# Kernel tuning notes

Measured on AMD Instinct MI355X. Metric: run time of the kernel, lower is better.

Reference implementation:

```python
import jax, jax.numpy as jnp
import numpy as np

EPS = 1e-5

def _layernorm(x, w, b):
    mu = jnp.mean(x, axis=-1, keepdims=True)
    var = jnp.mean(jnp.square(x - mu), axis=-1, keepdims=True)
    return (x - mu) * jax.lax.rsqrt(var + EPS) * w + b

def setup_inputs() -> dict:
    key = jax.random.key(0)
    ks = jax.random.split(key, 8)
    B, N, NH, F_IN, F_OUT = 1, 196608, 9, 64, 64
    x = jax.random.normal(ks[0], (B, N, F_IN), dtype=jnp.float32)
    adjc = jax.random.randint(ks[1], (N, NH), 0, N, dtype=jnp.int64)
    # NHConv layer weights: contract over (neighborhood, features)
    s1 = 1.0 / np.sqrt(NH * F_IN)
    s2 = 1.0 / np.sqrt(NH * F_OUT)
    W1 = jax.random.normal(ks[2], (NH, F_IN, F_OUT), dtype=jnp.float32) * s1
    b1 = jnp.zeros((F_OUT,), dtype=jnp.float32)
    W2 = jax.random.normal(ks[3], (NH, F_OUT, F_OUT), dtype=jnp.float32) * s2
    b2 = jnp.zeros((F_OUT,), dtype=jnp.float32)
    ln1_w = jnp.ones((F_IN,), dtype=jnp.float32)
    ln1_b = jnp.zeros((F_IN,), dtype=jnp.float32)
    ln2_w = jnp.ones((F_OUT,), dtype=jnp.float32)
    ln2_b = jnp.zeros((F_OUT,), dtype=jnp.float32)
    return {"x": x, "adjc": adjc, "ln1_w": ln1_w, "ln1_b": ln1_b,
            "W1": W1, "b1": b1, "ln2_w": ln2_w, "ln2_b": ln2_b,
            "W2": W2, "b2": b2}

def reference(x, adjc, ln1_w, ln1_b, W1, b1, ln2_w, ln2_b, W2, b2):
    # skip_layer: identity since in_features == out_features
    x_res = x
    # block 1: norm -> SiLU -> neighborhood gather -> per-node linear
    h = jax.nn.silu(_layernorm(x, ln1_w, ln1_b))
    h_nh = h[:, adjc, :]                      # [B, N, nh, F_in]
    h = jnp.einsum('bnkf,kfo->bno', h_nh, W1) + b1
    # block 2
    h = jax.nn.silu(_layernorm(h, ln2_w, ln2_b))
    h_nh = h[:, adjc, :]                      # [B, N, nh, F_out]
    h = jnp.einsum('bnkf,kfo->bno', h_nh, W2) + b2
    return h + x_res
```

## Files before the change

### kernel.cpp

```cpp
#include <hip/hip_runtime.h>

#define NNODES 196608
#define NH 9
#define F 64
#define K_TOT 576
#define KSTEPS 18
#define LN_EPS 1e-5f

typedef __attribute__((ext_vector_type(8))) short short8v;
typedef __attribute__((ext_vector_type(4))) float f32x4;

__device__ __forceinline__ unsigned short f2bf(float f) {
    unsigned int u = __float_as_uint(f);
    u += 0x7fff + ((u >> 16) & 1);
    return (unsigned short)(u >> 16);
}
__device__ __forceinline__ float bf2f(unsigned short u) {
    return __uint_as_float((unsigned int)u << 16);
}
__device__ __forceinline__ float silu_f(float z) { return z / (1.0f + __expf(-z)); }

__device__ __forceinline__ void gload_lds16(const void* g, void* l) {
    __builtin_amdgcn_global_load_lds((__attribute__((address_space(1))) void*)g,
                                     (__attribute__((address_space(3))) void*)l,
                                     16, 0, 0);
}

__global__ __launch_bounds__(256) void prep_wt(const float* __restrict__ W1,
                                               const float* __restrict__ W2,
                                               unsigned short* __restrict__ Wt1,
                                               unsigned short* __restrict__ Wt2) {
    int tid = blockIdx.x * 256 + threadIdx.x;
    if (tid >= F * K_TOT) return;
    int o = tid & 63, k = tid >> 6;
    int s = k >> 5, lg = (k & 31) >> 3, j = k & 7;
    int w = o >> 4, l16 = o & 15;
    int dst = ((s * 4 + w) * 64 + lg * 16 + l16) * 8 + j;
    Wt1[dst] = f2bf(W1[(size_t)k * F + o]);
    Wt2[dst] = f2bf(W2[(size_t)k * F + o]);
}

__global__ __launch_bounds__(256) void ln1_silu(const float* __restrict__ x,
                                                const float* __restrict__ w,
                                                const float* __restrict__ b,
                                                unsigned short* __restrict__ out,
                                                unsigned short* __restrict__ xbf) {
    const int t = threadIdx.x;
    const int row = blockIdx.x * 16 + (t >> 4);
    const int fl = (t & 15) * 4;
    const float4 v = *(const float4*)(x + (size_t)row * F + fl);
    float s = v.x + v.y + v.z + v.w;
    float ss = v.x * v.x + v.y * v.y + v.z * v.z + v.w * v.w;
#pragma unroll
    for (int o = 8; o; o >>= 1) { s += __shfl_xor(s, o); ss += __shfl_xor(ss, o); }
    const float mu = s * (1.0f / F);
    const float rstd = rsqrtf(ss * (1.0f / F) - mu * mu + LN_EPS);
    const float4 wv = *(const float4*)(w + fl);
    const float4 bv = *(const float4*)(b + fl);
    ushort4 o4;
    o4.x = f2bf(silu_f((v.x - mu) * rstd * wv.x + bv.x));
    o4.y = f2bf(silu_f((v.y - mu) * rstd * wv.y + bv.y));
    o4.z = f2bf(silu_f((v.z - mu) * rstd * wv.z + bv.z));
    o4.w = f2bf(silu_f((v.w - mu) * rstd * wv.w + bv.w));
    *(ushort4*)(out + (size_t)row * F + fl) = o4;
    if (xbf) {
        ushort4 xq;
        xq.x = f2bf(v.x); xq.y = f2bf(v.y); xq.z = f2bf(v.z); xq.w = f2bf(v.w);
        *(ushort4*)(xbf + (size_t)row * F + fl) = xq;
    }
}

template<int FINAL, int XBF>
__global__ __launch_bounds__(256) __attribute__((amdgpu_waves_per_eu(3, 4)))
void gconv_mfma(
    const unsigned short* __restrict__ h,
    const int* __restrict__ adjc,
    const unsigned short* __restrict__ Wt,
    const float* __restrict__ bias,
    const float* __restrict__ lnw, const float* __restrict__ lnb,
    const void* __restrict__ xres,
    void* __restrict__ outv)
{
    __shared__ __align__(16) char smem[4 * 8192];
    unsigned short* tile = (unsigned short*)smem;
    float (*T)[68] = (float (*)[68])smem;

    const int wave = threadIdx.x >> 6;
    const int lane = threadIdx.x & 63;
    const int l16 = lane & 15, lg = lane >> 4;
    const int nodeBase = blockIdx.x * 64;

    const int srow = lane >> 3;
    const int sswz = (lane & 7) ^ srow;
    const int rA = wave * 16 + srow;
    const int rB = rA + 8;

    int idxA[NH], idxB[NH];
    {
        const int* a0 = adjc + (size_t)(nodeBase + rA) * NH;
        const int* a1 = adjc + (size_t)(nodeBase + rB) * NH;
#pragma unroll
        for (int hh = 0; hh < NH; ++hh) { idxA[hh] = a0[hh]; idxB[hh] = a1[hh]; }
    }

    short8v bfrag[KSTEPS];
    {
        const short8v* wp = (const short8v*)(Wt) + (size_t)wave * 64 + lane;
#pragma unroll
        for (int s = 0; s < KSTEPS; ++s) bfrag[s] = wp[(size_t)s * 256];
    }
#pragma unroll
    for (int s = 0; s < KSTEPS; ++s)
        asm volatile("" : "+v"(bfrag[s]));

    f32x4 acc[4];
#pragma unroll
    for (int m = 0; m < 4; ++m) acc[m] = (f32x4){0.f, 0.f, 0.f, 0.f};

#define STAGE(BUF, HH)                                                         \
    do {                                                                       \
        gload_lds16(h + (size_t)idxA[HH] * F + sswz * 8,                       \
                    (char*)tile + (BUF) * 8192 + (2 * wave) * 1024);           \
        gload_lds16(h + (size_t)idxB[HH] * F + sswz * 8,                       \
                    (char*)tile + (BUF) * 8192 + (2 * wave + 1) * 1024);       \
    } while (0)

#define COMPUTE(BUF, HH)                                                       \
    _Pragma("unroll")                                                          \
    for (int m = 0; m < 4; ++m) {                                              \
        _Pragma("unroll")                                                      \
        for (int kh = 0; kh < 2; ++kh) {                                       \
            const short8v a = *(const short8v*)((char*)tile + (BUF) * 8192     \
                + (m * 16 + l16) * 128 + (((kh * 4 + lg) ^ (l16 & 7)) * 16));  \
            acc[m] = __builtin_amdgcn_mfma_f32_16x16x32_bf16(                  \
                a, bfrag[(HH) * 2 + kh], acc[m], 0, 0, 0);                     \
        }                                                                      \
    }

    STAGE(0, 0);
    STAGE(1, 1);
    STAGE(2, 2);
#pragma unroll
    for (int hh = 0; hh < NH; ++hh) {
        if (hh <= NH - 3)      { asm volatile("s_waitcnt vmcnt(4)" ::: "memory"); }
        else if (hh == NH - 2) { asm volatile("s_waitcnt vmcnt(2)" ::: "memory"); }
        else                   { asm volatile("s_waitcnt vmcnt(0)" ::: "memory"); }
        __builtin_amdgcn_s_barrier();
        if (hh < NH - 3) STAGE((hh + 3) & 3, hh + 3);
        COMPUTE(hh & 3, hh);
    }
#undef STAGE
#undef COMPUTE

    __syncthreads();

#pragma unroll
    for (int m = 0; m < 4; ++m)
#pragma unroll
        for (int r = 0; r < 4; ++r)
            T[m * 16 + lg * 4 + r][wave * 16 + l16] = acc[m][r];
    __syncthreads();

    const int t = threadIdx.x;
    const int nl = t >> 2, q = t & 3;
    const int node = nodeBase + nl;
    float v[16];
#pragma unroll
    for (int i = 0; i < 16; ++i) v[i] = T[nl][q * 16 + i] + bias[q * 16 + i];

    if (FINAL) {
        float* out = (float*)outv;
        if (XBF) {
            const unsigned short* xb = (const unsigned short*)xres;
            unsigned short xr[16];
            *(short8v*)(xr)     = *(const short8v*)(xb + (size_t)node * F + q * 16);
            *(short8v*)(xr + 8) = *(const short8v*)(xb + (size_t)node * F + q * 16 + 8);
#pragma unroll
            for (int i4 = 0; i4 < 4; ++i4) {
                float4 ov;
                ov.x = v[i4 * 4 + 0] + bf2f(xr[i4 * 4 + 0]);
                ov.y = v[i4 * 4 + 1] + bf2f(xr[i4 * 4 + 1]);
                ov.z = v[i4 * 4 + 2] + bf2f(xr[i4 * 4 + 2]);
                ov.w = v[i4 * 4 + 3] + bf2f(xr[i4 * 4 + 3]);
                *(float4*)(out + (size_t)node * F + q * 16 + i4 * 4) = ov;
            }
        } else {
            const float* xf = (const float*)xres;
#pragma unroll
            for (int i4 = 0; i4 < 4; ++i4) {
                const float4 xv = *(const float4*)(xf + (size_t)node * F + q * 16 + i4 * 4);
                float4 ov;
                ov.x = v[i4 * 4 + 0] + xv.x; ov.y = v[i4 * 4 + 1] + xv.y;
                ov.z = v[i4 * 4 + 2] + xv.z; ov.w = v[i4 * 4 + 3] + xv.w;
                *(float4*)(out + (size_t)node * F + q * 16 + i4 * 4) = ov;
            }
        }
    } else {
        float s = 0.f, ss = 0.f;
#pragma unroll
        for (int i = 0; i < 16; ++i) { s += v[i]; ss += v[i] * v[i]; }
        s += __shfl_xor(s, 1); ss += __shfl_xor(ss, 1);
        s += __shfl_xor(s, 2); ss += __shfl_xor(ss, 2);
        const float mu = s * (1.0f / F);
        const float rstd = rsqrtf(ss * (1.0f / F) - mu * mu + LN_EPS);
        unsigned short* out = (unsigned short*)outv;
        unsigned short ob[16];
#pragma unroll
        for (int i = 0; i < 16; ++i) {
            const int o = q * 16 + i;
            const float y = (v[i] - mu) * rstd * lnw[o] + lnb[o];
            ob[i] = f2bf(silu_f(y));
        }
#pragma unroll
        for (int c = 0; c < 2; ++c)
            *(short8v*)(out + (size_t)node * F + q * 16 + c * 8) = *(short8v*)(ob + c * 8);
    }
}

extern "C" void kernel_launch(void* const* d_in, const int* in_sizes, int n_in,
                              void* d_out, int out_size, void* d_ws, size_t ws_size,
                              hipStream_t stream)
{
    const float* x    = (const float*)d_in[0];
    const int*   adjc = (const int*)d_in[1];
    const float* ln1w = (const float*)d_in[2];
    const float* ln1b = (const float*)d_in[3];
    const float* W1   = (const float*)d_in[4];
    const float* b1   = (const float*)d_in[5];
    const float* ln2w = (const float*)d_in[6];
    const float* ln2b = (const float*)d_in[7];
    const float* W2   = (const float*)d_in[8];
    const float* b2   = (const float*)d_in[9];
    float* out = (float*)d_out;

    const size_t hElems = (size_t)NNODES * F;
    unsigned short* h1  = (unsigned short*)d_ws;
    unsigned short* h2  = h1 + hElems;
    unsigned short* Wt1 = h2 + hElems;
    unsigned short* Wt2 = Wt1 + F * K_TOT;
    unsigned short* xbf = Wt2 + F * K_TOT;
    const size_t need = (3 * hElems + 2 * (size_t)F * K_TOT) * sizeof(unsigned short);
    const bool useXbf = ws_size >= need;

    prep_wt<<<(F * K_TOT + 255) / 256, 256, 0, stream>>>(W1, W2, Wt1, Wt2);
    ln1_silu<<<NNODES / 16, 256, 0, stream>>>(x, ln1w, ln1b, h1, useXbf ? xbf : nullptr);
    gconv_mfma<0, 0><<<NNODES / 64, 256, 0, stream>>>(h1, adjc, Wt1, b1, ln2w, ln2b, nullptr, h2);
    if (useXbf)
        gconv_mfma<1, 1><<<NNODES / 64, 256, 0, stream>>>(h2, adjc, Wt2, b2, nullptr, nullptr, xbf, out);
    else
        gconv_mfma<1, 0><<<NNODES / 64, 256, 0, stream>>>(h2, adjc, Wt2, b2, nullptr, nullptr, x, out);
}
```

Before: 108.6 us.

## Make each wave compute all output columns for its own 16 nodes without block barriers

Each wave now owns a private LDS region and 16 nodes, and computes all four 16-column output tiles itself, so the block-wide barriers in the gather loop go away. Weight fragments are no longer held in registers for the whole kernel; they are double-buffered per neighbor from global memory, interleaved with a four-deep gather pipeline driven by explicit vmcnt waits. The epilogue reads the MFMA accumulators directly and does the LayerNorm reduction with 16-lane shuffles, which drops the LDS transpose. In exchange, every wave re-reads the full weight matrix per neighbor, and the output writes become narrow scalar stores instead of vector stores. The waves-per-EU hint is also pinned to 3.

```diff
diff --git a/kernel.cpp b/kernel.cpp
--- a/kernel.cpp
+++ b/kernel.cpp
@@ -4,7 +4,6 @@
 #define NH 9
 #define F 64
 #define K_TOT 576
-#define KSTEPS 18
 #define LN_EPS 1e-5f
 
 typedef __attribute__((ext_vector_type(8))) short short8v;
@@ -71,7 +70,7 @@
 }
 
 template<int FINAL, int XBF>
-__global__ __launch_bounds__(256) __attribute__((amdgpu_waves_per_eu(3, 4)))
+__global__ __launch_bounds__(256) __attribute__((amdgpu_waves_per_eu(3, 3)))
 void gconv_mfma(
     const unsigned short* __restrict__ h,
     const int* __restrict__ adjc,
@@ -82,138 +81,127 @@
     void* __restrict__ outv)
 {
     __shared__ __align__(16) char smem[4 * 8192];
-    unsigned short* tile = (unsigned short*)smem;
-    float (*T)[68] = (float (*)[68])smem;
-
-    const int wave = threadIdx.x >> 6;
+    char* wreg = smem + (threadIdx.x >> 6) * 8192;
+
     const int lane = threadIdx.x & 63;
     const int l16 = lane & 15, lg = lane >> 4;
-    const int nodeBase = blockIdx.x * 64;
+    const int base = blockIdx.x * 64 + (threadIdx.x >> 6) * 16;
 
     const int srow = lane >> 3;
     const int sswz = (lane & 7) ^ srow;
-    const int rA = wave * 16 + srow;
-    const int rB = rA + 8;
-
-    int idxA[NH], idxB[NH];
+
+    int sidx0[NH], sidx1[NH];
     {
-        const int* a0 = adjc + (size_t)(nodeBase + rA) * NH;
-        const int* a1 = adjc + (size_t)(nodeBase + rB) * NH;
-#pragma unroll
-        for (int hh = 0; hh < NH; ++hh) { idxA[hh] = a0[hh]; idxB[hh] = a1[hh]; }
+        const int* a0 = adjc + (size_t)(base + srow) * NH;
+        const int* a1 = adjc + (size_t)(base + 8 + srow) * NH;
+#pragma unroll
+        for (int hh = 0; hh < NH; ++hh) { sidx0[hh] = a0[hh]; sidx1[hh] = a1[hh]; }
     }
 
-    short8v bfrag[KSTEPS];
-    {
-        const short8v* wp = (const short8v*)(Wt) + (size_t)wave * 64 + lane;
-#pragma unroll
-        for (int s = 0; s < KSTEPS; ++s) bfrag[s] = wp[(size_t)s * 256];
-    }
-#pragma unroll
-    for (int s = 0; s < KSTEPS; ++s)
-        asm volatile("" : "+v"(bfrag[s]));
-
     f32x4 acc[4];
 #pragma unroll
-    for (int m = 0; m < 4; ++m) acc[m] = (f32x4){0.f, 0.f, 0.f, 0.f};
-
-#define STAGE(BUF, HH)                                                         \
-    do {                                                                       \
-        gload_lds16(h + (size_t)idxA[HH] * F + sswz * 8,                       \
-                    (char*)tile + (BUF) * 8192 + (2 * wave) * 1024);           \
-        gload_lds16(h + (size_t)idxB[HH] * F + sswz * 8,                       \
-                    (char*)tile + (BUF) * 8192 + (2 * wave + 1) * 1024);       \
+    for (int ot = 0; ot < 4; ++ot) acc[ot] = (f32x4){0.f, 0.f, 0.f, 0.f};
+
+    short8v Bp[2][4][2];
+
+#define STAGE(BUF, HH) do {                                                    \
+        gload_lds16(h + (size_t)sidx0[HH] * F + sswz * 8, wreg + (BUF) * 2048);\
+        gload_lds16(h + (size_t)sidx1[HH] * F + sswz * 8,                      \
+                    wreg + (BUF) * 2048 + 1024);                               \
     } while (0)
 
-#define COMPUTE(BUF, HH)                                                       \
-    _Pragma("unroll")                                                          \
-    for (int m = 0; m < 4; ++m) {                                              \
-        _Pragma("unroll")                                                      \
-        for (int kh = 0; kh < 2; ++kh) {                                       \
-            const short8v a = *(const short8v*)((char*)tile + (BUF) * 8192     \
-                + (m * 16 + l16) * 128 + (((kh * 4 + lg) ^ (l16 & 7)) * 16));  \
-            acc[m] = __builtin_amdgcn_mfma_f32_16x16x32_bf16(                  \
-                a, bfrag[(HH) * 2 + kh], acc[m], 0, 0, 0);                     \
-        }                                                                      \
-    }
-
-    STAGE(0, 0);
-    STAGE(1, 1);
-    STAGE(2, 2);
-#pragma unroll
-    for (int hh = 0; hh < NH; ++hh) {
-        if (hh <= NH - 3)      { asm volatile("s_waitcnt vmcnt(4)" ::: "memory"); }
-        else if (hh == NH - 2) { asm volatile("s_waitcnt vmcnt(2)" ::: "memory"); }
-        else                   { asm volatile("s_waitcnt vmcnt(0)" ::: "memory"); }
-        __builtin_amdgcn_s_barrier();
-        if (hh < NH - 3) STAGE((hh + 3) & 3, hh + 3);
-        COMPUTE(hh & 3, hh);
-    }
+#define BLOAD(P, HH) do {                                                      \
+        const short8v* wq = (const short8v*)Wt + (size_t)(HH) * 512 + lane;    \
+        Bp[P][0][0] = wq[0];   Bp[P][1][0] = wq[64];                           \
+        Bp[P][2][0] = wq[128]; Bp[P][3][0] = wq[192];                          \
+        Bp[P][0][1] = wq[256]; Bp[P][1][1] = wq[320];                          \
+        Bp[P][2][1] = wq[384]; Bp[P][3][1] = wq[448];                          \
+    } while (0)
+
+#define COMPUTE(BUF, P) do {                                                   \
+        const short8v a0v = *(const short8v*)(wreg + (BUF) * 2048              \
+            + l16 * 128 + ((lg ^ (l16 & 7)) * 16));                            \
+        const short8v a1v = *(const short8v*)(wreg + (BUF) * 2048              \
+            + l16 * 128 + (((4 + lg) ^ (l16 & 7)) * 16));                      \
+        acc[0] = __builtin_amdgcn_mfma_f32_16x16x32_bf16(a0v, Bp[P][0][0], acc[0], 0, 0, 0); \
+        acc[1] = __builtin_amdgcn_mfma_f32_16x16x32_bf16(a0v, Bp[P][1][0], acc[1], 0, 0, 0); \
+        acc[2] = __builtin_amdgcn_mfma_f32_16x16x32_bf16(a0v, Bp[P][2][0], acc[2], 0, 0, 0); \
+        acc[3] = __builtin_amdgcn_mfma_f32_16x16x32_bf16(a0v, Bp[P][3][0], acc[3], 0, 0, 0); \
+        acc[0] = __builtin_amdgcn_mfma_f32_16x16x32_bf16(a1v, Bp[P][0][1], acc[0], 0, 0, 0); \
+        acc[1] = __builtin_amdgcn_mfma_f32_16x16x32_bf16(a1v, Bp[P][1][1], acc[1], 0, 0, 0); \
+        acc[2] = __builtin_amdgcn_mfma_f32_16x16x32_bf16(a1v, Bp[P][2][1], acc[2], 0, 0, 0); \
+        acc[3] = __builtin_amdgcn_mfma_f32_16x16x32_bf16(a1v, Bp[P][3][1], acc[3], 0, 0, 0); \
+    } while (0)
+
+#define VW(N) asm volatile("s_waitcnt vmcnt(" #N ")" ::: "memory")
+
+    STAGE(0, 0); STAGE(1, 1); STAGE(2, 2); BLOAD(0, 0);
+    STAGE(3, 3); BLOAD(1, 1); VW(10); COMPUTE(0, 0);
+    STAGE(0, 4); BLOAD(0, 2); VW(10); COMPUTE(1, 1);
+    STAGE(1, 5); BLOAD(1, 3); VW(10); COMPUTE(2, 0);
+    STAGE(2, 6); BLOAD(0, 4); VW(10); COMPUTE(3, 1);
+    STAGE(3, 7); BLOAD(1, 5); VW(10); COMPUTE(0, 0);
+    STAGE(0, 8); BLOAD(0, 6); VW(10); COMPUTE(1, 1);
+    BLOAD(1, 7);              VW(8);  COMPUTE(2, 0);
+    BLOAD(0, 8);              VW(8);  COMPUTE(3, 1);
+                              VW(0);  COMPUTE(0, 0);
 #undef STAGE
+#undef BLOAD
 #undef COMPUTE
-
-    __syncthreads();
-
-#pragma unroll
-    for (int m = 0; m < 4; ++m)
-#pragma unroll
-        for (int r = 0; r < 4; ++r)
-            T[m * 16 + lg * 4 + r][wave * 16 + l16] = acc[m][r];
-    __syncthreads();
-
-    const int t = threadIdx.x;
-    const int nl = t >> 2, q = t & 3;
-    const int node = nodeBase + nl;
-    float v[16];
-#pragma unroll
-    for (int i = 0; i < 16; ++i) v[i] = T[nl][q * 16 + i] + bias[q * 16 + i];
+#undef VW
+
+    float vbias[4];
+#pragma unroll
+    for (int ot = 0; ot < 4; ++ot) vbias[ot] = bias[ot * 16 + l16];
 
     if (FINAL) {
         float* out = (float*)outv;
-        if (XBF) {
-            const unsigned short* xb = (const unsigned short*)xres;
-            unsigned short xr[16];
-            *(short8v*)(xr)     = *(const short8v*)(xb + (size_t)node * F + q * 16);
-            *(short8v*)(xr + 8) = *(const short8v*)(xb + (size_t)node * F + q * 16 + 8);
-#pragma unroll
-            for (int i4 = 0; i4 < 4; ++i4) {
-                float4 ov;
-                ov.x = v[i4 * 4 + 0] + bf2f(xr[i4 * 4 + 0]);
-                ov.y = v[i4 * 4 + 1] + bf2f(xr[i4 * 4 + 1]);
-                ov.z = v[i4 * 4 + 2] + bf2f(xr[i4 * 4 + 2]);
-                ov.w = v[i4 * 4 + 3] + bf2f(xr[i4 * 4 + 3]);
-                *(float4*)(out + (size_t)node * F + q * 16 + i4 * 4) = ov;
-            }
-        } else {
-            const float* xf = (const float*)xres;
-#pragma unroll
-            for (int i4 = 0; i4 < 4; ++i4) {
-                const float4 xv = *(const float4*)(xf + (size_t)node * F + q * 16 + i4 * 4);
-                float4 ov;
-                ov.x = v[i4 * 4 + 0] + xv.x; ov.y = v[i4 * 4 + 1] + xv.y;
-                ov.z = v[i4 * 4 + 2] + xv.z; ov.w = v[i4 * 4 + 3] + xv.w;
-                *(float4*)(out + (size_t)node * F + q * 16 + i4 * 4) = ov;
+#pragma unroll
+        for (int r = 0; r < 4; ++r) {
+            const int node = base + lg * 4 + r;
+            if (XBF) {
+                const unsigned short* xb = (const unsigned short*)xres;
+#pragma unroll
+                for (int ot = 0; ot < 4; ++ot) {
+                    const int o = ot * 16 + l16;
+                    out[(size_t)node * F + o] =
+                        acc[ot][r] + vbias[ot] + bf2f(xb[(size_t)node * F + o]);
+                }
+            } else {
+                const float* xf = (const float*)xres;
+#pragma unroll
+                for (int ot = 0; ot < 4; ++ot) {
+                    const int o = ot * 16 + l16;
+                    out[(size_t)node * F + o] =
+                        acc[ot][r] + vbias[ot] + xf[(size_t)node * F + o];
+                }
             }
         }
     } else {
-        float s = 0.f, ss = 0.f;
-#pragma unroll
-        for (int i = 0; i < 16; ++i) { s += v[i]; ss += v[i] * v[i]; }
-        s += __shfl_xor(s, 1); ss += __shfl_xor(ss, 1);
-        s += __shfl_xor(s, 2); ss += __shfl_xor(ss, 2);
-        const float mu = s * (1.0f / F);
-        const float rstd = rsqrtf(ss * (1.0f / F) - mu * mu + LN_EPS);
+        float lw[4], lb[4];
+#pragma unroll
+        for (int ot = 0; ot < 4; ++ot) { lw[ot] = lnw[ot * 16 + l16]; lb[ot] = lnb[ot * 16 + l16]; }
         unsigned short* out = (unsigned short*)outv;
-        unsigned short ob[16];
-#pragma unroll
-        for (int i = 0; i < 16; ++i) {
-            const int o = q * 16 + i;
-            const float y = (v[i] - mu) * rstd * lnw[o] + lnb[o];
-            ob[i] = f2bf(silu_f(y));
+#pragma unroll
+        for (int r = 0; r < 4; ++r) {
+            const float v0 = acc[0][r] + vbias[0];
+            const float v1 = acc[1][r] + vbias[1];
+            const float v2 = acc[2][r] + vbias[2];
+            const float v3 = acc[3][r] + vbias[3];
+            float s  = v0 + v1 + v2 + v3;
+            float ss = v0 * v0 + v1 * v1 + v2 * v2 + v3 * v3;
+            s += __shfl_xor(s, 1); ss += __shfl_xor(ss, 1);
+            s += __shfl_xor(s, 2); ss += __shfl_xor(ss, 2);
+            s += __shfl_xor(s, 4); ss += __shfl_xor(ss, 4);
+            s += __shfl_xor(s, 8); ss += __shfl_xor(ss, 8);
+            const float mu = s * (1.0f / F);
+            const float rstd = rsqrtf(ss * (1.0f / F) - mu * mu + LN_EPS);
+            const int node = base + lg * 4 + r;
+            out[(size_t)node * F +  0 + l16] = f2bf(silu_f((v0 - mu) * rstd * lw[0] + lb[0]));
+            out[(size_t)node * F + 16 + l16] = f2bf(silu_f((v1 - mu) * rstd * lw[1] + lb[1]));
+            out[(size_t)node * F + 32 + l16] = f2bf(silu_f((v2 - mu) * rstd * lw[2] + lb[2]));
+            out[(size_t)node * F + 48 + l16] = f2bf(silu_f((v3 - mu) * rstd * lw[3] + lb[3]));
         }
-#pragma unroll
-        for (int c = 0; c < 2; ++c)
-            *(short8v*)(out + (size_t)node * F + q * 16 + c * 8) = *(short8v*)(ob + c * 8);
     }
 }
 
```

Result: slower. 200.5 us (+84.6%).
